# Optimization experiments

Hardware: AMD Instinct MI355X
Metric: run time of the kernel (lower is better)

## Reference

```python
import jax, jax.numpy as jnp
import numpy as np

T = 4194304  # sequence length (2**22)

def setup_inputs() -> dict:
    key = jax.random.key(0)
    k = jax.random.split(key, 7)
    return {
        "x_0": jax.random.normal(k[0], (1, 2), dtype=jnp.float32),
        "u": jax.random.normal(k[1], (2, T), dtype=jnp.float32),
        "timedelta": jax.random.uniform(k[2], (T,), dtype=jnp.float32),
        # scale W_A down so the linear recurrence x_t = A x_{t-1} + ... is stable over 4M steps
        "W_A": 0.3 * jax.random.normal(k[3], (2, 2), dtype=jnp.float32),
        "b_A": 0.1 * jax.random.normal(k[4], (2,), dtype=jnp.float32),
        "W_B": jax.random.normal(k[5], (2, 2), dtype=jnp.float32),
        "b_B": 0.1 * jax.random.normal(k[6], (2,), dtype=jnp.float32),
    }

def reference(x_0, u, timedelta, W_A, b_A, W_B, b_B):
    # forward_PINN: linear state recurrence x_t = A x_{t-1} + B u_t (+biases),
    # output_t = physics_prediction(x_{t-1}, u_t, dt_t) - x_t
    x0 = x_0[0]          # [2] state (x, y)
    u_seq = u.T          # [T, 2] controls (speed, heading)

    def step(x_prev, inp):
        u_t, dt = inp                                  # [2], scalar
        x_t = W_A @ x_prev + b_A + W_B @ u_t + b_B     # [2]
        c = u_t[0] * dt
        pinn = x_prev + jnp.stack([c * jnp.cos(u_t[1]), c * jnp.sin(u_t[1])])
        return x_t, pinn - x_t

    _, x_out = jax.lax.scan(step, x0, (u_seq, timedelta))  # [T, 2]
    return x_out
```

## Files before the change

kernel.cpp:

```cpp
#include <hip/hip_runtime.h>

#define T_TOTAL 4194304
#define S 16
#define NTHREADS 256
#define BLOCK_T (NTHREADS * S)
#define WPB 2
#define HALO_SEG 4
#define NSEG (NTHREADS + HALO_SEG)

struct M22 { float m00, m01, m10, m11; };
__device__ __forceinline__ M22 mmul(const M22& X, const M22& Y) {
    M22 r;
    r.m00 = fmaf(X.m00, Y.m00, X.m01 * Y.m10);
    r.m01 = fmaf(X.m00, Y.m01, X.m01 * Y.m11);
    r.m10 = fmaf(X.m10, Y.m00, X.m11 * Y.m10);
    r.m11 = fmaf(X.m10, Y.m01, X.m11 * Y.m11);
    return r;
}

struct alignas(16) F16 { float f[16]; };
__device__ __forceinline__ void load16(F16& d, const float* __restrict__ p) {
    const float4* q = (const float4*)p;
    float4 a0 = q[0], a1 = q[1], a2 = q[2], a3 = q[3];
    *(float4*)&d.f[0]  = a0;
    *(float4*)&d.f[4]  = a1;
    *(float4*)&d.f[8]  = a2;
    *(float4*)&d.f[12] = a3;
}

__global__ __launch_bounds__(NTHREADS, 2)
void pinn_rnn_kernel(const float* __restrict__ x0p,
                     const float* __restrict__ u,
                     const float* __restrict__ td,
                     const float* __restrict__ WA,
                     const float* __restrict__ bA,
                     const float* __restrict__ WB,
                     const float* __restrict__ bB,
                     float* __restrict__ out)
{
    __shared__ float2 lc0[NSEG], lc1[NSEG];
    __shared__ float2 lout0[BLOCK_T], lout1[BLOCK_T];

    const int tid = threadIdx.x;
    const int B0  = blockIdx.x * (WPB * BLOCK_T);
    const int B1  = B0 + BLOCK_T;

    const float a00 = WA[0], a01 = WA[1], a10 = WA[2], a11 = WA[3];
    const float w00 = WB[0], w01 = WB[1], w10 = WB[2], w11 = WB[3];
    const float bc0 = bA[0] + bB[0];
    const float bc1 = bA[1] + bB[1];

    const float* u0 = u;
    const float* u1 = u + T_TOTAL;

    const int t0 = B0 + tid * S;
    F16 U0a, U1a, DTa;
    load16(U0a, u0 + t0);
    load16(U1a, u1 + t0);
    load16(DTa, td + t0);

    F16 H0, H1;
    float X0 = 0.f, X1 = 0.f;
    const bool halo_owner = (tid < HALO_SEG);
    if (halo_owner) {
        if (blockIdx.x != 0) {
            const int th = B0 - HALO_SEG * S + tid * S;
            load16(H0, u0 + th);
            load16(H1, u1 + th);
        } else {
            X0 = x0p[0]; X1 = x0p[1];
            #pragma unroll
            for (int o = 0; o < 4; ++o) { *(float4*)&H0.f[o*4] = make_float4(0,0,0,0);
                                          *(float4*)&H1.f[o*4] = make_float4(0,0,0,0); }
        }
    }

    M22 A   = { a00, a01, a10, a11 };
    M22 A2  = mmul(A,  A );
    M22 A4  = mmul(A2, A2);
    M22 A8  = mmul(A4, A4);
    M22 M   = mmul(A8, A8);
    M22 Mp2 = mmul(M,  M );
    M22 Mp3 = mmul(Mp2, M);

    {
        float x0v = 0.f, x1v = 0.f;
        #pragma unroll
        for (int j = 0; j < S; ++j) {
            float v0 = fmaf(w00, U0a.f[j], fmaf(w01, U1a.f[j], bc0));
            float v1 = fmaf(w10, U0a.f[j], fmaf(w11, U1a.f[j], bc1));
            float n0 = fmaf(a00, x0v, fmaf(a01, x1v, v0));
            float n1 = fmaf(a10, x0v, fmaf(a11, x1v, v1));
            x0v = n0; x1v = n1;
        }
        lc0[tid + HALO_SEG] = make_float2(x0v, x1v);
    }
    if (halo_owner) {
        float x0v = 0.f, x1v = 0.f;
        #pragma unroll
        for (int j = 0; j < S; ++j) {
            float v0 = fmaf(w00, H0.f[j], fmaf(w01, H1.f[j], bc0));
            float v1 = fmaf(w10, H0.f[j], fmaf(w11, H1.f[j], bc1));
            float n0 = fmaf(a00, x0v, fmaf(a01, x1v, v0));
            float n1 = fmaf(a10, x0v, fmaf(a11, x1v, v1));
            x0v = n0; x1v = n1;
        }
        lc0[tid] = make_float2(x0v, x1v);
        if (blockIdx.x == 0) lc0[tid] = make_float2(0.f, 0.f);
    }

    const int t1 = B1 + tid * S;
    F16 U0b, U1b, DTb;
    load16(U0b, u0 + t1);
    load16(U1b, u1 + t1);
    load16(DTb, td + t1);

    __syncthreads();

    if (halo_owner) lc1[tid] = lc0[NTHREADS + tid];

    {
        float2 c1 = lc0[tid + 3], c2 = lc0[tid + 2], c3 = lc0[tid + 1], c4 = lc0[tid];
        float xi0 = c1.x
                  + fmaf(M.m00,   c2.x, M.m01   * c2.y)
                  + fmaf(Mp2.m00, c3.x, Mp2.m01 * c3.y)
                  + fmaf(Mp3.m00, c4.x, Mp3.m01 * c4.y);
        float xi1 = c1.y
                  + fmaf(M.m10,   c2.x, M.m11   * c2.y)
                  + fmaf(Mp2.m10, c3.x, Mp2.m11 * c3.y)
                  + fmaf(Mp3.m10, c4.x, Mp3.m11 * c4.y);
        if (blockIdx.x == 0 && halo_owner) {
            M22 P;
            if      (tid == 0) P = { 1.f, 0.f, 0.f, 1.f };
            else if (tid == 1) P = M;
            else if (tid == 2) P = Mp2;
            else               P = Mp3;
            xi0 += fmaf(P.m00, X0, P.m01 * X1);
            xi1 += fmaf(P.m10, X0, P.m11 * X1);
        }
        const int xm = tid & 14;
        float2* lrow = lout0 + tid * S;
        float x0v = xi0, x1v = xi1;
        #pragma unroll
        for (int j = 0; j < S; ++j) {
            float v0 = fmaf(w00, U0a.f[j], fmaf(w01, U1a.f[j], bc0));
            float v1 = fmaf(w10, U0a.f[j], fmaf(w11, U1a.f[j], bc1));
            float n0 = fmaf(a00, x0v, fmaf(a01, x1v, v0));
            float n1 = fmaf(a10, x0v, fmaf(a11, x1v, v1));
            float cc = U0a.f[j] * DTa.f[j];
            float sn, cs;
            __sincosf(U1a.f[j], &sn, &cs);
            lrow[j ^ xm] = make_float2(fmaf(cc, cs, x0v) - n0,
                                       fmaf(cc, sn, x1v) - n1);
            x0v = n0; x1v = n1;
        }
    }
    __syncthreads();

    {
        const float4* lo4 = (const float4*)lout0;
        float4* og = (float4*)out + (B0 >> 1);
        #pragma unroll
        for (int m = 0; m < 8; ++m) {
            int f    = m * NTHREADS + tid;
            int i0   = f << 1;
            int slot = i0 ^ ((i0 >> 4) & 14);
            og[f] = lo4[slot >> 1];
        }
    }
    {
        float x0v = 0.f, x1v = 0.f;
        #pragma unroll
        for (int j = 0; j < S; ++j) {
            float v0 = fmaf(w00, U0b.f[j], fmaf(w01, U1b.f[j], bc0));
            float v1 = fmaf(w10, U0b.f[j], fmaf(w11, U1b.f[j], bc1));
            float n0 = fmaf(a00, x0v, fmaf(a01, x1v, v0));
            float n1 = fmaf(a10, x0v, fmaf(a11, x1v, v1));
            x0v = n0; x1v = n1;
        }
        lc1[tid + HALO_SEG] = make_float2(x0v, x1v);
    }
    __syncthreads();

    {
        float2 c1 = lc1[tid + 3], c2 = lc1[tid + 2], c3 = lc1[tid + 1], c4 = lc1[tid];
        float xi0 = c1.x
                  + fmaf(M.m00,   c2.x, M.m01   * c2.y)
                  + fmaf(Mp2.m00, c3.x, Mp2.m01 * c3.y)
                  + fmaf(Mp3.m00, c4.x, Mp3.m01 * c4.y);
        float xi1 = c1.y
                  + fmaf(M.m10,   c2.x, M.m11   * c2.y)
                  + fmaf(Mp2.m10, c3.x, Mp2.m11 * c3.y)
                  + fmaf(Mp3.m10, c4.x, Mp3.m11 * c4.y);
        const int xm = tid & 14;
        float2* lrow = lout1 + tid * S;
        float x0v = xi0, x1v = xi1;
        #pragma unroll
        for (int j = 0; j < S; ++j) {
            float v0 = fmaf(w00, U0b.f[j], fmaf(w01, U1b.f[j], bc0));
            float v1 = fmaf(w10, U0b.f[j], fmaf(w11, U1b.f[j], bc1));
            float n0 = fmaf(a00, x0v, fmaf(a01, x1v, v0));
            float n1 = fmaf(a10, x0v, fmaf(a11, x1v, v1));
            float cc = U0b.f[j] * DTb.f[j];
            float sn, cs;
            __sincosf(U1b.f[j], &sn, &cs);
            lrow[j ^ xm] = make_float2(fmaf(cc, cs, x0v) - n0,
                                       fmaf(cc, sn, x1v) - n1);
            x0v = n0; x1v = n1;
        }
    }
    __syncthreads();

    {
        const float4* lo4 = (const float4*)lout1;
        float4* og = (float4*)out + (B1 >> 1);
        #pragma unroll
        for (int m = 0; m < 8; ++m) {
            int f    = m * NTHREADS + tid;
            int i0   = f << 1;
            int slot = i0 ^ ((i0 >> 4) & 14);
            og[f] = lo4[slot >> 1];
        }
    }
}

extern "C" void kernel_launch(void* const* d_in, const int* in_sizes, int n_in,
                              void* d_out, int out_size, void* d_ws, size_t ws_size,
                              hipStream_t stream) {
    const float* x0p = (const float*)d_in[0];
    const float* u   = (const float*)d_in[1];
    const float* td  = (const float*)d_in[2];
    const float* WA  = (const float*)d_in[3];
    const float* bA  = (const float*)d_in[4];
    const float* WB  = (const float*)d_in[5];
    const float* bB  = (const float*)d_in[6];
    float* outp = (float*)d_out;

    dim3 grid(T_TOTAL / (WPB * BLOCK_T));
    dim3 block(NTHREADS);
    pinn_rnn_kernel<<<grid, block, 0, stream>>>(x0p, u, td, WA, bA, WB, bB, outp);
}
```

Measured before the change: 105.2 us.

## Process one tile per block and raise occupancy target to four blocks

Drops the two-tiles-per-block scheme. Each block now handles one 4096-step tile and recomputes its own 4-segment halo instead of reusing the previous tile's carries. This halves shared memory and registers per block, and the launch bound goes from 2 to 4 blocks per CU so more waves can hide memory latency. In exchange, the grid doubles to 1024 blocks and the halo recomputation is done twice as often, and the prefetch of the second tile, which overlapped with the first tile's compute, is lost.

```diff
diff --git a/kernel.cpp b/kernel.cpp
--- a/kernel.cpp
+++ b/kernel.cpp
@@ -4,7 +4,6 @@
 #define S 16
 #define NTHREADS 256
 #define BLOCK_T (NTHREADS * S)
-#define WPB 2
 #define HALO_SEG 4
 #define NSEG (NTHREADS + HALO_SEG)
 
@@ -28,7 +27,7 @@
     *(float4*)&d.f[12] = a3;
 }
 
-__global__ __launch_bounds__(NTHREADS, 2)
+__global__ __launch_bounds__(NTHREADS, 4)
 void pinn_rnn_kernel(const float* __restrict__ x0p,
                      const float* __restrict__ u,
                      const float* __restrict__ td,
@@ -38,12 +37,11 @@
                      const float* __restrict__ bB,
                      float* __restrict__ out)
 {
-    __shared__ float2 lc0[NSEG], lc1[NSEG];
-    __shared__ float2 lout0[BLOCK_T], lout1[BLOCK_T];
+    __shared__ float2 lc[NSEG];
+    __shared__ float2 lout[BLOCK_T];
 
     const int tid = threadIdx.x;
-    const int B0  = blockIdx.x * (WPB * BLOCK_T);
-    const int B1  = B0 + BLOCK_T;
+    const int B0  = blockIdx.x * BLOCK_T;
 
     const float a00 = WA[0], a01 = WA[1], a10 = WA[2], a11 = WA[3];
     const float w00 = WB[0], w01 = WB[1], w10 = WB[2], w11 = WB[3];
@@ -69,9 +67,6 @@
             load16(H1, u1 + th);
         } else {
             X0 = x0p[0]; X1 = x0p[1];
-            #pragma unroll
-            for (int o = 0; o < 4; ++o) { *(float4*)&H0.f[o*4] = make_float4(0,0,0,0);
-                                          *(float4*)&H1.f[o*4] = make_float4(0,0,0,0); }
         }
     }
 
@@ -93,34 +88,29 @@
             float n1 = fmaf(a10, x0v, fmaf(a11, x1v, v1));
             x0v = n0; x1v = n1;
         }
-        lc0[tid + HALO_SEG] = make_float2(x0v, x1v);
+        lc[tid + HALO_SEG] = make_float2(x0v, x1v);
     }
     if (halo_owner) {
-        float x0v = 0.f, x1v = 0.f;
-        #pragma unroll
-        for (int j = 0; j < S; ++j) {
-            float v0 = fmaf(w00, H0.f[j], fmaf(w01, H1.f[j], bc0));
-            float v1 = fmaf(w10, H0.f[j], fmaf(w11, H1.f[j], bc1));
-            float n0 = fmaf(a00, x0v, fmaf(a01, x1v, v0));
-            float n1 = fmaf(a10, x0v, fmaf(a11, x1v, v1));
-            x0v = n0; x1v = n1;
+        if (blockIdx.x != 0) {
+            float x0v = 0.f, x1v = 0.f;
+            #pragma unroll
+            for (int j = 0; j < S; ++j) {
+                float v0 = fmaf(w00, H0.f[j], fmaf(w01, H1.f[j], bc0));
+                float v1 = fmaf(w10, H0.f[j], fmaf(w11, H1.f[j], bc1));
+                float n0 = fmaf(a00, x0v, fmaf(a01, x1v, v0));
+                float n1 = fmaf(a10, x0v, fmaf(a11, x1v, v1));
+                x0v = n0; x1v = n1;
+            }
+            lc[tid] = make_float2(x0v, x1v);
+        } else {
+            lc[tid] = make_float2(0.f, 0.f);
         }
-        lc0[tid] = make_float2(x0v, x1v);
-        if (blockIdx.x == 0) lc0[tid] = make_float2(0.f, 0.f);
     }
-
-    const int t1 = B1 + tid * S;
-    F16 U0b, U1b, DTb;
-    load16(U0b, u0 + t1);
-    load16(U1b, u1 + t1);
-    load16(DTb, td + t1);
 
     __syncthreads();
 
-    if (halo_owner) lc1[tid] = lc0[NTHREADS + tid];
-
     {
-        float2 c1 = lc0[tid + 3], c2 = lc0[tid + 2], c3 = lc0[tid + 1], c4 = lc0[tid];
+        float2 c1 = lc[tid + 3], c2 = lc[tid + 2], c3 = lc[tid + 1], c4 = lc[tid];
         float xi0 = c1.x
                   + fmaf(M.m00,   c2.x, M.m01   * c2.y)
                   + fmaf(Mp2.m00, c3.x, Mp2.m01 * c3.y)
@@ -139,7 +129,7 @@
             xi1 += fmaf(P.m10, X0, P.m11 * X1);
         }
         const int xm = tid & 14;
-        float2* lrow = lout0 + tid * S;
+        float2* lrow = lout + tid * S;
         float x0v = xi0, x1v = xi1;
         #pragma unroll
         for (int j = 0; j < S; ++j) {
@@ -158,62 +148,8 @@
     __syncthreads();
 
     {
-        const float4* lo4 = (const float4*)lout0;
+        const float4* lo4 = (const float4*)lout;
         float4* og = (float4*)out + (B0 >> 1);
-        #pragma unroll
-        for (int m = 0; m < 8; ++m) {
-            int f    = m * NTHREADS + tid;
-            int i0   = f << 1;
-            int slot = i0 ^ ((i0 >> 4) & 14);
-            og[f] = lo4[slot >> 1];
-        }
-    }
-    {
-        float x0v = 0.f, x1v = 0.f;
-        #pragma unroll
-        for (int j = 0; j < S; ++j) {
-            float v0 = fmaf(w00, U0b.f[j], fmaf(w01, U1b.f[j], bc0));
-            float v1 = fmaf(w10, U0b.f[j], fmaf(w11, U1b.f[j], bc1));
-            float n0 = fmaf(a00, x0v, fmaf(a01, x1v, v0));
-            float n1 = fmaf(a10, x0v, fmaf(a11, x1v, v1));
-            x0v = n0; x1v = n1;
-        }
-        lc1[tid + HALO_SEG] = make_float2(x0v, x1v);
-    }
-    __syncthreads();
-
-    {
-        float2 c1 = lc1[tid + 3], c2 = lc1[tid + 2], c3 = lc1[tid + 1], c4 = lc1[tid];
-        float xi0 = c1.x
-                  + fmaf(M.m00,   c2.x, M.m01   * c2.y)
-                  + fmaf(Mp2.m00, c3.x, Mp2.m01 * c3.y)
-                  + fmaf(Mp3.m00, c4.x, Mp3.m01 * c4.y);
-        float xi1 = c1.y
-                  + fmaf(M.m10,   c2.x, M.m11   * c2.y)
-                  + fmaf(Mp2.m10, c3.x, Mp2.m11 * c3.y)
-                  + fmaf(Mp3.m10, c4.x, Mp3.m11 * c4.y);
-        const int xm = tid & 14;
-        float2* lrow = lout1 + tid * S;
-        float x0v = xi0, x1v = xi1;
-        #pragma unroll
-        for (int j = 0; j < S; ++j) {
-            float v0 = fmaf(w00, U0b.f[j], fmaf(w01, U1b.f[j], bc0));
-            float v1 = fmaf(w10, U0b.f[j], fmaf(w11, U1b.f[j], bc1));
-            float n0 = fmaf(a00, x0v, fmaf(a01, x1v, v0));
-            float n1 = fmaf(a10, x0v, fmaf(a11, x1v, v1));
-            float cc = U0b.f[j] * DTb.f[j];
-            float sn, cs;
-            __sincosf(U1b.f[j], &sn, &cs);
-            lrow[j ^ xm] = make_float2(fmaf(cc, cs, x0v) - n0,
-                                       fmaf(cc, sn, x1v) - n1);
-            x0v = n0; x1v = n1;
-        }
-    }
-    __syncthreads();
-
-    {
-        const float4* lo4 = (const float4*)lout1;
-        float4* og = (float4*)out + (B1 >> 1);
         #pragma unroll
         for (int m = 0; m < 8; ++m) {
             int f    = m * NTHREADS + tid;
@@ -236,7 +172,7 @@
     const float* bB  = (const float*)d_in[6];
     float* outp = (float*)d_out;
 
-    dim3 grid(T_TOTAL / (WPB * BLOCK_T));
+    dim3 grid(T_TOTAL / BLOCK_T);
     dim3 block(NTHREADS);
     pinn_rnn_kernel<<<grid, block, 0, stream>>>(x0p, u, td, WA, bA, WB, bB, outp);
 }
```

Measured after the change: 105.4 us. Within noise of the previous version (+0.2%).
